# Kernel optimization log

Hardware: AMD Instinct MI355X
Metric: run time of the kernel (lower is better)

Reference implementation:

```python
import jax, jax.numpy as jnp
import numpy as np
from jax import lax

ALPHA = 0.2  # LeakyReLU negative slope
PAD = 1      # circular padding


def conv1d_circular(x, w, b):
    # x: [M, C, F], w: [O, C, K], b: [O]; circular padding, stride 1
    xp = jnp.pad(x, ((0, 0), (0, 0), (PAD, PAD)), mode='wrap')
    y = lax.conv_general_dilated(xp, w, window_strides=(1,), padding='VALID',
                                 dimension_numbers=('NCH', 'OIH', 'NCH'))
    return y + b[None, :, None]


def setup_inputs() -> dict:
    key = jax.random.key(0)
    ks = jax.random.split(key, 6)
    B, N, C, F = 8, 1024, 64, 32
    O = 128
    return {
        'x': jax.random.normal(ks[0], (B, N, C, F), dtype=jnp.float32),
        'n': jax.random.normal(ks[1], (B, N, C, F), dtype=jnp.float32),
        'conv_w': jax.random.normal(ks[2], (O, C, 3), dtype=jnp.float32) * 0.05,
        'conv_b': jax.random.normal(ks[3], (O,), dtype=jnp.float32) * 0.05,
        'att1_w': jax.random.normal(ks[4], (1, O * F), dtype=jnp.float32) * 0.02,
        'att2_w': jax.random.normal(ks[5], (1, O * F), dtype=jnp.float32) * 0.02,
    }


def reference(x, n, conv_w, conv_b, att1_w, att2_w):
    B, N, C, F = x.shape
    O = conv_w.shape[0]
    h1 = conv1d_circular(x.reshape(B * N, C, F), conv_w, conv_b).reshape(B, N, O * F)
    h2 = conv1d_circular(n.reshape(B * N, C, F), conv_w, conv_b).reshape(B, N, O * F)
    a1 = jnp.einsum('bnd,od->bno', h1, att1_w)  # [B,N,1]
    a2 = jnp.einsum('bnd,od->bno', h2, att2_w)  # [B,N,1]
    a = a1 + jnp.swapaxes(a2, -1, -2)           # [B,N,N]
    a = jnp.where(a >= 0, a, ALPHA * a)         # LeakyReLU
    att = jax.nn.softmax(a, axis=1)             # softmax over dim=1 as in torch
    out = jnp.einsum('bij,bjd->bid', att, h1)   # [B,N,O*F]
    return out.reshape(B, N, O, F)
```

## Files before the change

### kernel.cpp

```cpp
#include <hip/hip_runtime.h>


#define ALPHA 0.2f
typedef __attribute__((ext_vector_type(8))) short short8;
typedef __attribute__((ext_vector_type(4))) float f32x4;

constexpr int Bb = 8, Nn = 1024, Cc = 64, Ff = 32, Oo = 128, Dd = 4096, Mm = 8192;

__device__ __forceinline__ unsigned short f2bf(float v) {
  unsigned int u = __float_as_uint(v);
  unsigned int r = (u + 0x7FFFu + ((u >> 16) & 1u)) >> 16;
  return (unsigned short)r;
}
__device__ __forceinline__ float bf2f(unsigned short h) {
  return __uint_as_float(((unsigned int)h) << 16);
}

__global__ __launch_bounds__(256) void prep_kernel(
    const float* __restrict__ w, const float* __restrict__ bias,
    const float* __restrict__ att1w, const float* __restrict__ att2w,
    unsigned short* __restrict__ Bph, unsigned short* __restrict__ Bpl,
    float* __restrict__ W1, float* __restrict__ W2, float* __restrict__ c12) {
  const int tid = threadIdx.x;
  const int gid = blockIdx.x * 256 + tid;
  for (int e = gid; e < 6 * 8 * 64 * 8; e += 64 * 256) {
    int j = e & 7, l = (e >> 3) & 63, ot = (e >> 9) & 7, kc = e >> 12;
    int kn = kc * 32 + ((l >> 4) << 3) + j;
    int c = kn & 63, k = kn >> 6;
    int o = ot * 16 + (l & 15);
    float v = w[o * 192 + c * 3 + k];
    unsigned short hi = f2bf(v);
    Bph[e] = hi;
    Bpl[e] = f2bf(v - bf2f(hi));
  }
  if (gid < 4096) {
    int which = gid >> 11;
    int e = gid & 2047;
    int c = e >> 5, g = e & 31;
    const float* aw = which ? att2w : att1w;
    float s = 0.f;
    for (int o = 0; o < 128; ++o) {
      const float* wp = w + o * 192 + c * 3;
      const float* ap = aw + o * 32;
#pragma unroll
      for (int k = 0; k < 3; ++k) s += wp[k] * ap[(g - k + 1 + 32) & 31];
    }
    (which ? W2 : W1)[e] = s;
  }
  if (blockIdx.x == 63) {
    __shared__ float red[256];
    int o = tid & 127;
    const float* aw = (tid < 128) ? att1w : att2w;
    float t = 0.f;
    for (int f = 0; f < 32; ++f) t += aw[o * 32 + f];
    red[tid] = t * bias[o];
    __syncthreads();
    for (int st = 64; st >= 1; st >>= 1) {
      if ((tid & 127) < st) red[tid] += red[tid + st];
      __syncthreads();
    }
    if (tid == 0) c12[0] = red[0];
    if (tid == 128) c12[1] = red[128];
  }
}

__global__ __launch_bounds__(256) void a12_kernel(
    const float* __restrict__ x, const float* __restrict__ n,
    const float* __restrict__ W1, const float* __restrict__ W2,
    const float* __restrict__ c12, float* __restrict__ a1,
    float* __restrict__ a2, float* __restrict__ segsum) {
  const int tid = threadIdx.x, lane = tid & 63, wv = tid >> 6;
  const int gid = blockIdx.x * 256 + tid;
  segsum[(size_t)gid * 2] = 0.f;
  segsum[(size_t)gid * 2 + 1] = 0.f;
  float4 w1r[8], w2r[8];
#pragma unroll
  for (int q = 0; q < 8; ++q) {
    w1r[q] = *reinterpret_cast<const float4*>(W1 + q * 256 + lane * 4);
    w2r[q] = *reinterpret_cast<const float4*>(W2 + q * 256 + lane * 4);
  }
  const float c1 = c12[0], c2v = c12[1];
  const int gw = blockIdx.x * 4 + wv;
#pragma unroll
  for (int rr = 0; rr < 2; ++rr) {
    int m = gw * 2 + rr;
    const float* xp = x + (size_t)m * 2048;
    const float* np = n + (size_t)m * 2048;
    float s1 = 0.f, s2 = 0.f;
#pragma unroll
    for (int q = 0; q < 8; ++q) {
      float4 xv = *reinterpret_cast<const float4*>(xp + q * 256 + lane * 4);
      float4 nv = *reinterpret_cast<const float4*>(np + q * 256 + lane * 4);
      s1 += w1r[q].x * xv.x + w1r[q].y * xv.y + w1r[q].z * xv.z + w1r[q].w * xv.w;
      s2 += w2r[q].x * nv.x + w2r[q].y * nv.y + w2r[q].z * nv.z + w2r[q].w * nv.w;
    }
#pragma unroll
    for (int d = 1; d < 64; d <<= 1) {
      s1 += __shfl_xor(s1, d);
      s2 += __shfl_xor(s2, d);
    }
    if (lane == 0) { a1[m] = s1 + c1; a2[m] = s2 + c2v; }
  }
}

__global__ __launch_bounds__(1024) void sortprep_kernel(
    const float* __restrict__ a1, const float* __restrict__ a2,
    float* __restrict__ jsu, float* __restrict__ jsv, int* __restrict__ jrow,
    int* __restrict__ isrow, int* __restrict__ isk,
    float* __restrict__ isep, float* __restrict__ isea) {
  __shared__ float k1[1024]; __shared__ int x1[1024];
  __shared__ float k2[1024]; __shared__ int x2[1024];
  __shared__ float p1[1024]; __shared__ float q1[1024];
  const int tid = threadIdx.x;
  const int b = blockIdx.x;
  k1[tid] = a1[b * 1024 + tid]; x1[tid] = tid;
  k2[tid] = a2[b * 1024 + tid]; x2[tid] = tid;
  __syncthreads();
  for (int k = 2; k <= 1024; k <<= 1) {
    for (int j = k >> 1; j > 0; j >>= 1) {
      int ixj = tid ^ j;
      if (ixj > tid) {
        bool up = ((tid & k) == 0);
        float va = k1[tid], vb = k1[ixj];
        if ((va > vb) == up) {
          k1[tid] = vb; k1[ixj] = va;
          int t = x1[tid]; x1[tid] = x1[ixj]; x1[ixj] = t;
        }
        float wa = k2[tid], wb = k2[ixj];
        if ((wa > wb) == up) {
          k2[tid] = wb; k2[ixj] = wa;
          int t = x2[tid]; x2[tid] = x2[ixj]; x2[ixj] = t;
        }
      }
      __syncthreads();
    }
  }
  p1[tid] = expf(k1[tid]);
  q1[tid] = expf(ALPHA * k1[tid]);
  __syncthreads();
  for (int off = 1; off < 1024; off <<= 1) {
    float ap = (tid >= off) ? p1[tid - off] : 0.f;
    float aq = (tid >= off) ? q1[tid - off] : 0.f;
    __syncthreads();
    p1[tid] += ap; q1[tid] += aq;
    __syncthreads();
  }
  const float Ptot = p1[1023];
  {
    float a2v = k2[tid];
    float thr = -a2v;
    int lo = 0, hi = 1024;
    while (lo < hi) { int mid = (lo + hi) >> 1; if (k1[mid] < thr) lo = mid + 1; else hi = mid; }
    float Psuf = Ptot - (lo ? p1[lo - 1] : 0.f);
    float Qpre = lo ? q1[lo - 1] : 0.f;
    float eb = expf(a2v), ea = expf(ALPHA * a2v);
    float den = eb * Psuf + ea * Qpre;
    jsu[b * 1024 + tid] = eb / den;
    jsv[b * 1024 + tid] = ea / den;
    jrow[b * 1024 + tid] = b * 1024 + x2[tid];
  }
  {
    float a1v = k1[tid];
    float thr = -a1v;
    int lo = 0, hi = 1024;
    while (lo < hi) { int mid = (lo + hi) >> 1; if (k2[mid] < thr) lo = mid + 1; else hi = mid; }
    int s = 1023 - tid;
    isrow[b * 1024 + s] = b * 1024 + x1[tid];
    isk[b * 1024 + s] = lo;
    isep[b * 1024 + s] = expf(a1v);
    isea[b * 1024 + s] = expf(ALPHA * a1v);
  }
}

__global__ __launch_bounds__(256, 2) void conv_kernel(
    const float* __restrict__ x,
    const unsigned short* __restrict__ Bph, const unsigned short* __restrict__ Bpl,
    const float* __restrict__ bias,
    const int* __restrict__ jrow, const float* __restrict__ jsu,
    const float* __restrict__ jsv,
    float* __restrict__ h1s, float* __restrict__ segsum) {
  __shared__ unsigned char xsraw[16384];
  const int tid = threadIdx.x, lane = tid & 63, wv = tid >> 6;
  const int s0 = blockIdx.x * 16;

  short8 bh[6][2], bl[6][2];
#pragma unroll
  for (int kc = 0; kc < 6; ++kc)
#pragma unroll
    for (int t2 = 0; t2 < 2; ++t2) {
      int ot = wv * 2 + t2;
      size_t idx = ((size_t)(kc * 8 + ot) * 64 + lane) * 8;
      bh[kc][t2] = *reinterpret_cast<const short8*>(Bph + idx);
      bl[kc][t2] = *reinterpret_cast<const short8*>(Bpl + idx);
    }
  float biasv[2];
  biasv[0] = bias[(wv * 2 + 0) * 16 + (lane & 15)];
  biasv[1] = bias[(wv * 2 + 1) * 16 + (lane & 15)];

  int offs[2][6];
#pragma unroll
  for (int ft = 0; ft < 2; ++ft)
#pragma unroll
    for (int kc = 0; kc < 6; ++kc) {
      int fo = ft * 16 + (lane & 15);
      int kb = kc * 32 + ((lane >> 4) << 3);
      int k = kb >> 6, c0 = kb & 63;
      int fx = (fo + k + 31) & 31;
      int bo = (fx << 7) + (c0 << 1);
      offs[ft][kc] = bo ^ ((fx & 7) << 4);
    }

  float Uacc[2][2][4] = {{{0.f}}};
  float Vacc[2][2][4] = {{{0.f}}};
  const int cpair = tid & 31, fq = tid >> 5;

  auto stage = [&](int r, int bf) {
    int m = jrow[s0 + r];
    const float* xr = x + (size_t)m * 2048;
    int c = cpair * 2;
    float4 v0 = *reinterpret_cast<const float4*>(xr + c * 32 + fq * 4);
    float4 v1 = *reinterpret_cast<const float4*>(xr + (c + 1) * 32 + fq * 4);
    unsigned char* base = xsraw + bf * 8192;
#pragma unroll
    for (int ff = 0; ff < 4; ++ff) {
      int f = fq * 4 + ff;
      float av = (&v0.x)[ff], bv = (&v1.x)[ff];
      unsigned short ah = f2bf(av), bh_ = f2bf(bv);
      unsigned short al = f2bf(av - bf2f(ah)), bl_ = f2bf(bv - bf2f(bh_));
      int bo = ((f << 7) + (c << 1)) ^ ((f & 7) << 4);
      *reinterpret_cast<unsigned int*>(base + bo) =
          (unsigned int)ah | ((unsigned int)bh_ << 16);
      *reinterpret_cast<unsigned int*>(base + 4096 + bo) =
          (unsigned int)al | ((unsigned int)bl_ << 16);
    }
  };

  stage(0, 0);
  __syncthreads();
  for (int r = 0; r < 16; ++r) {
    if (r < 15) stage(r + 1, (r + 1) & 1);
    const unsigned char* bufb = xsraw + (r & 1) * 8192;
    f32x4 acc[2][2];
#pragma unroll
    for (int ft = 0; ft < 2; ++ft)
#pragma unroll
      for (int t2 = 0; t2 < 2; ++t2) {
        f32x4 z = {0.f, 0.f, 0.f, 0.f};
        acc[ft][t2] = z;
      }
#pragma unroll
    for (int kc = 0; kc < 6; ++kc) {
#pragma unroll
      for (int ft = 0; ft < 2; ++ft) {
        short8 ah = *reinterpret_cast<const short8*>(bufb + offs[ft][kc]);
        short8 al = *reinterpret_cast<const short8*>(bufb + 4096 + offs[ft][kc]);
        acc[ft][0] = __builtin_amdgcn_mfma_f32_16x16x32_bf16(ah, bh[kc][0], acc[ft][0], 0, 0, 0);
        acc[ft][1] = __builtin_amdgcn_mfma_f32_16x16x32_bf16(ah, bh[kc][1], acc[ft][1], 0, 0, 0);
        acc[ft][0] = __builtin_amdgcn_mfma_f32_16x16x32_bf16(ah, bl[kc][0], acc[ft][0], 0, 0, 0);
        acc[ft][1] = __builtin_amdgcn_mfma_f32_16x16x32_bf16(ah, bl[kc][1], acc[ft][1], 0, 0, 0);
        acc[ft][0] = __builtin_amdgcn_mfma_f32_16x16x32_bf16(al, bh[kc][0], acc[ft][0], 0, 0, 0);
        acc[ft][1] = __builtin_amdgcn_mfma_f32_16x16x32_bf16(al, bh[kc][1], acc[ft][1], 0, 0, 0);
      }
    }
    const int s = s0 + r;
    const float ju = jsu[s], jv = jsv[s];
    float* hrow = h1s + (size_t)s * 4096;
#pragma unroll
    for (int ft = 0; ft < 2; ++ft)
#pragma unroll
      for (int t2 = 0; t2 < 2; ++t2) {
        int f_base = ft * 16 + ((lane >> 4) << 2);
        int o_out = (wv * 2 + t2) * 16 + (lane & 15);
        float4 hv;
#pragma unroll
        for (int reg = 0; reg < 4; ++reg) {
          float val = acc[ft][t2][reg] + biasv[t2];
          (&hv.x)[reg] = val;
          Uacc[ft][t2][reg] += ju * val;
          Vacc[ft][t2][reg] += jv * val;
        }
        *reinterpret_cast<float4*>(hrow + o_out * 32 + f_base) = hv;
      }
    __syncthreads();
  }
  const int g = blockIdx.x >> 3;
  float* su = segsum + (size_t)g * 2 * 4096;
#pragma unroll
  for (int ft = 0; ft < 2; ++ft)
#pragma unroll
    for (int t2 = 0; t2 < 2; ++t2)
#pragma unroll
      for (int reg = 0; reg < 4; ++reg) {
        int col = ((wv * 2 + t2) * 16 + (lane & 15)) * 32 + ft * 16 +
                  ((lane >> 4) << 2) + reg;
        atomicAdd(su + col, Uacc[ft][t2][reg]);
        atomicAdd(su + 4096 + col, Vacc[ft][t2][reg]);
      }
}

__global__ __launch_bounds__(128) void pass2_kernel(
    const float* __restrict__ h1s, const float* __restrict__ segsum,
    const float* __restrict__ jsu, const float* __restrict__ jsv,
    const int* __restrict__ isrow, const int* __restrict__ isk,
    const float* __restrict__ isep, const float* __restrict__ isea,
    float* __restrict__ out) {
  const int tid = threadIdx.x;
  const int chunk = blockIdx.x & 31, gseg = blockIdx.x >> 5;
  const int b = gseg >> 3, seg = gseg & 7;
  const int col = chunk * 128 + tid;
  __shared__ int kL[1024];
  __shared__ float epL[1024];
  __shared__ float eaL[1024];
  __shared__ int rowL[1024];
  __shared__ float juL[128];
  __shared__ float jvL[128];
  for (int i = tid; i < 1024; i += 128) {
    kL[i] = isk[b * 1024 + i];
    epL[i] = isep[b * 1024 + i];
    eaL[i] = isea[b * 1024 + i];
    rowL[i] = isrow[b * 1024 + i];
  }
  juL[tid] = jsu[b * 1024 + seg * 128 + tid];
  jvL[tid] = jsv[b * 1024 + seg * 128 + tid];
  float U = 0.f, V = 0.f, Utot = 0.f;
#pragma unroll
  for (int s8 = 0; s8 < 8; ++s8) {
    float uu = segsum[((size_t)(b * 8 + s8) * 2) * 4096 + col];
    float vv = segsum[((size_t)(b * 8 + s8) * 2 + 1) * 4096 + col];
    Utot += uu;
    if (s8 < seg) { U += uu; V += vv; }
  }
  __syncthreads();
  int ip, ip1;
  {
    int lo = 0, hi = 1024, thr = seg * 128;
    while (lo < hi) { int mid = (lo + hi) >> 1; if (kL[mid] < thr) lo = mid + 1; else hi = mid; }
    ip = lo;
  }
  if (seg == 7) ip1 = 1024;
  else {
    int lo = ip, hi = 1024, thr = seg * 128 + 128;
    while (lo < hi) { int mid = (lo + hi) >> 1; if (kL[mid] < thr) lo = mid + 1; else hi = mid; }
    ip1 = lo;
  }
  const float* hrow = h1s + ((size_t)(b * 1024 + seg * 128)) * 4096 + col;
  for (int t = 0; t < 128; t += 16) {
    float rr[16];
#pragma unroll
    for (int q = 0; q < 16; ++q) rr[q] = hrow[(size_t)(t + q) * 4096];
#pragma unroll
    for (int q = 0; q < 16; ++q) {
      int cnt = seg * 128 + t + q;
      while (ip < ip1 && kL[ip] <= cnt) {
        out[(size_t)rowL[ip] * 4096 + col] = epL[ip] * (Utot - U) + eaL[ip] * V;
        ++ip;
      }
      U += juL[t + q] * rr[q];
      V += jvL[t + q] * rr[q];
    }
  }
  while (ip < ip1) {
    out[(size_t)rowL[ip] * 4096 + col] = epL[ip] * (Utot - U) + eaL[ip] * V;
    ++ip;
  }
}

extern "C" void kernel_launch(void* const* d_in, const int* in_sizes, int n_in,
                              void* d_out, int out_size, void* d_ws, size_t ws_size,
                              hipStream_t stream) {
  const float* x     = (const float*)d_in[0];
  const float* n     = (const float*)d_in[1];
  const float* w     = (const float*)d_in[2];
  const float* bias  = (const float*)d_in[3];
  const float* att1w = (const float*)d_in[4];
  const float* att2w = (const float*)d_in[5];
  float* out = (float*)d_out;
  float* wsf = (float*)d_ws;

  size_t off = 0;
  float* h1s  = wsf + off; off += (size_t)Mm * Dd;
  float* W1   = wsf + off; off += 2048;
  float* W2   = wsf + off; off += 2048;
  float* c12  = wsf + off; off += 64;
  float* a1v  = wsf + off; off += Mm;
  float* a2v  = wsf + off; off += Mm;
  float* jsu  = wsf + off; off += Mm;
  float* jsv  = wsf + off; off += Mm;
  int*   jrow = (int*)(wsf + off); off += Mm;
  int*   isrow= (int*)(wsf + off); off += Mm;
  int*   isk  = (int*)(wsf + off); off += Mm;
  float* isep = wsf + off; off += Mm;
  float* isea = wsf + off; off += Mm;
  float* segsum = wsf + off; off += (size_t)64 * 2 * 4096;
  unsigned short* Bph = (unsigned short*)(wsf + off); off += 12288;
  unsigned short* Bpl = (unsigned short*)(wsf + off); off += 12288;

  prep_kernel<<<64, 256, 0, stream>>>(w, bias, att1w, att2w, Bph, Bpl, W1, W2, c12);
  a12_kernel<<<1024, 256, 0, stream>>>(x, n, W1, W2, c12, a1v, a2v, segsum);
  sortprep_kernel<<<Bb, 1024, 0, stream>>>(a1v, a2v, jsu, jsv, jrow,
                                           isrow, isk, isep, isea);
  conv_kernel<<<512, 256, 0, stream>>>(x, Bph, Bpl, bias, jrow, jsu, jsv,
                                       h1s, segsum);
  pass2_kernel<<<2048, 128, 0, stream>>>(h1s, segsum, jsu, jsv,
                                         isrow, isk, isep, isea, out);
}
```

Measured before the change: 411.1 us.

## Replace bitonic sort with rank sort, wave-shuffle scan, and double conv grid

```diff
diff --git a/kernel.cpp b/kernel.cpp
--- a/kernel.cpp
+++ b/kernel.cpp
@@ -108,43 +108,54 @@
     float* __restrict__ jsu, float* __restrict__ jsv, int* __restrict__ jrow,
     int* __restrict__ isrow, int* __restrict__ isk,
     float* __restrict__ isep, float* __restrict__ isea) {
+  __shared__ __align__(16) float A1[1024];
+  __shared__ __align__(16) float A2[1024];
   __shared__ float k1[1024]; __shared__ int x1[1024];
   __shared__ float k2[1024]; __shared__ int x2[1024];
   __shared__ float p1[1024]; __shared__ float q1[1024];
+  __shared__ float wp[16]; __shared__ float wq[16];
   const int tid = threadIdx.x;
+  const int lane = tid & 63, wv = tid >> 6;
   const int b = blockIdx.x;
-  k1[tid] = a1[b * 1024 + tid]; x1[tid] = tid;
-  k2[tid] = a2[b * 1024 + tid]; x2[tid] = tid;
-  __syncthreads();
-  for (int k = 2; k <= 1024; k <<= 1) {
-    for (int j = k >> 1; j > 0; j >>= 1) {
-      int ixj = tid ^ j;
-      if (ixj > tid) {
-        bool up = ((tid & k) == 0);
-        float va = k1[tid], vb = k1[ixj];
-        if ((va > vb) == up) {
-          k1[tid] = vb; k1[ixj] = va;
-          int t = x1[tid]; x1[tid] = x1[ixj]; x1[ixj] = t;
-        }
-        float wa = k2[tid], wb = k2[ixj];
-        if ((wa > wb) == up) {
-          k2[tid] = wb; k2[ixj] = wa;
-          int t = x2[tid]; x2[tid] = x2[ixj]; x2[ixj] = t;
-        }
-      }
-      __syncthreads();
-    }
-  }
-  p1[tid] = expf(k1[tid]);
-  q1[tid] = expf(ALPHA * k1[tid]);
-  __syncthreads();
-  for (int off = 1; off < 1024; off <<= 1) {
-    float ap = (tid >= off) ? p1[tid - off] : 0.f;
-    float aq = (tid >= off) ? q1[tid - off] : 0.f;
-    __syncthreads();
-    p1[tid] += ap; q1[tid] += aq;
-    __syncthreads();
-  }
+  const float v1 = a1[b * 1024 + tid];
+  const float v2 = a2[b * 1024 + tid];
+  A1[tid] = v1; A2[tid] = v2;
+  __syncthreads();
+  int r1 = 0, r2 = 0;
+  for (int j = 0; j < 1024; j += 4) {
+    float4 c1 = *reinterpret_cast<const float4*>(&A1[j]);
+    float4 c2 = *reinterpret_cast<const float4*>(&A2[j]);
+    r1 += (c1.x < v1 || (c1.x == v1 && j + 0 < tid)) ? 1 : 0;
+    r1 += (c1.y < v1 || (c1.y == v1 && j + 1 < tid)) ? 1 : 0;
+    r1 += (c1.z < v1 || (c1.z == v1 && j + 2 < tid)) ? 1 : 0;
+    r1 += (c1.w < v1 || (c1.w == v1 && j + 3 < tid)) ? 1 : 0;
+    r2 += (c2.x < v2 || (c2.x == v2 && j + 0 < tid)) ? 1 : 0;
+    r2 += (c2.y < v2 || (c2.y == v2 && j + 1 < tid)) ? 1 : 0;
+    r2 += (c2.z < v2 || (c2.z == v2 && j + 2 < tid)) ? 1 : 0;
+    r2 += (c2.w < v2 || (c2.w == v2 && j + 3 < tid)) ? 1 : 0;
+  }
+  k1[r1] = v1; x1[r1] = tid;
+  k2[r2] = v2; x2[r2] = tid;
+  __syncthreads();
+  float pv = expf(k1[tid]);
+  float qv = expf(ALPHA * k1[tid]);
+#pragma unroll
+  for (int off = 1; off < 64; off <<= 1) {
+    float tp = __shfl_up(pv, off);
+    float tq = __shfl_up(qv, off);
+    if (lane >= off) { pv += tp; qv += tq; }
+  }
+  if (lane == 63) { wp[wv] = pv; wq[wv] = qv; }
+  __syncthreads();
+  if (tid == 0) {
+    float sp = 0.f, sq = 0.f;
+#pragma unroll
+    for (int i = 0; i < 16; ++i) { sp += wp[i]; wp[i] = sp; sq += wq[i]; wq[i] = sq; }
+  }
+  __syncthreads();
+  if (wv > 0) { pv += wp[wv - 1]; qv += wq[wv - 1]; }
+  p1[tid] = pv; q1[tid] = qv;
+  __syncthreads();
   const float Ptot = p1[1023];
   {
     float a2v = k2[tid];
@@ -172,7 +183,7 @@
   }
 }
 
-__global__ __launch_bounds__(256, 2) void conv_kernel(
+__global__ __launch_bounds__(256, 4) void conv_kernel(
     const float* __restrict__ x,
     const unsigned short* __restrict__ Bph, const unsigned short* __restrict__ Bpl,
     const float* __restrict__ bias,
@@ -181,7 +192,7 @@
     float* __restrict__ h1s, float* __restrict__ segsum) {
   __shared__ unsigned char xsraw[16384];
   const int tid = threadIdx.x, lane = tid & 63, wv = tid >> 6;
-  const int s0 = blockIdx.x * 16;
+  const int s0 = blockIdx.x * 8;
 
   short8 bh[6][2], bl[6][2];
 #pragma unroll
@@ -237,8 +248,8 @@
 
   stage(0, 0);
   __syncthreads();
-  for (int r = 0; r < 16; ++r) {
-    if (r < 15) stage(r + 1, (r + 1) & 1);
+  for (int r = 0; r < 8; ++r) {
+    if (r < 7) stage(r + 1, (r + 1) & 1);
     const unsigned char* bufb = xsraw + (r & 1) * 8192;
     f32x4 acc[2][2];
 #pragma unroll
@@ -283,7 +294,7 @@
       }
     __syncthreads();
   }
-  const int g = blockIdx.x >> 3;
+  const int g = blockIdx.x >> 4;
   float* su = segsum + (size_t)g * 2 * 4096;
 #pragma unroll
   for (int ft = 0; ft < 2; ++ft)
@@ -399,8 +410,8 @@
   a12_kernel<<<1024, 256, 0, stream>>>(x, n, W1, W2, c12, a1v, a2v, segsum);
   sortprep_kernel<<<Bb, 1024, 0, stream>>>(a1v, a2v, jsu, jsv, jrow,
                                            isrow, isk, isep, isea);
-  conv_kernel<<<512, 256, 0, stream>>>(x, Bph, Bpl, bias, jrow, jsu, jsv,
-                                       h1s, segsum);
+  conv_kernel<<<Mm / 8, 256, 0, stream>>>(x, Bph, Bpl, bias, jrow, jsu, jsv,
+                                          h1s, segsum);
   pass2_kernel<<<2048, 128, 0, stream>>>(h1s, segsum, jsu, jsv,
                                          isrow, isk, isep, isea, out);
 }
```

New measurement: 558.6 us. +35.9%, slower.
